# Performance work log

Measured on AMD Instinct MI355X. Metric: run time of the kernel, lower is better.

## Reference

```python
import jax, jax.numpy as jnp
import numpy as np

S, B, MAX_IN, MAX_OUT = 2048, 32, 256, 80
MIN_IN = 20
EPS = 1e-5  # torch BatchNorm1d default


def setup_inputs() -> dict:
    key = jax.random.key(0)
    ks = jax.random.split(key, 4)
    # ragged gene-set sizes per subsystem, and DCell's output-size rule
    in_sizes = jax.random.randint(ks[0], (S,), MIN_IN, MAX_IN + 1)
    out_sizes = jnp.maximum(20, (0.3 * in_sizes).astype(jnp.int32))
    in_mask = (jnp.arange(MAX_IN)[None, :] < in_sizes[:, None]).astype(jnp.float32)   # [S, MAX_IN]
    out_mask = (jnp.arange(MAX_OUT)[None, :] < out_sizes[:, None]).astype(jnp.float32)  # [S, MAX_OUT]
    # gathered mutant states per subsystem (padded), [S, B, MAX_IN]
    x = jax.random.normal(ks[1], (S, B, MAX_IN), dtype=jnp.float32) * in_mask[:, None, :]
    # per-subsystem Linear params (stacked), Kaiming-ish scale
    W = jax.random.normal(ks[2], (S, MAX_OUT, MAX_IN), dtype=jnp.float32) / np.sqrt(MAX_IN).astype(np.float32)
    b = jax.random.normal(ks[3], (S, MAX_OUT), dtype=jnp.float32) * 0.01
    gamma = jnp.ones((S, MAX_OUT), dtype=jnp.float32)
    beta = jnp.zeros((S, MAX_OUT), dtype=jnp.float32)
    return {"x": x, "W": W, "b": b, "gamma": gamma, "beta": beta,
            "in_mask": in_mask, "out_mask": out_mask}


def reference(x, W, b, gamma, beta, in_mask, out_mask):
    # grouped Linear over all subsystems at once: [S,B,I] x [S,O,I] -> [S,B,O]
    xm = x * in_mask[:, None, :]
    h = jnp.einsum('sbi,soi->sbo', xm, W) + b[:, None, :]
    h = jnp.tanh(h)
    # BatchNorm1d (training mode): normalize over the batch dim per subsystem/feature
    mean = jnp.mean(h, axis=1, keepdims=True)
    var = jnp.mean(jnp.square(h - mean), axis=1, keepdims=True)  # biased, as torch BN uses
    y = (h - mean) * jax.lax.rsqrt(var + EPS) * gamma[:, None, :] + beta[:, None, :]
    # zero out padded output features
    return y * out_mask[:, None, :]
```

## Files before the change

kernel.cpp:

```cpp
#include <hip/hip_runtime.h>

#define S_TOT 2048
#define B_SZ  32
#define I_SZ  256
#define O_SZ  80

typedef _Float16 f16x8 __attribute__((ext_vector_type(8)));
typedef _Float16 f16x4 __attribute__((ext_vector_type(4)));
typedef float    f32x4 __attribute__((ext_vector_type(4)));

__global__ __launch_bounds__(320, 5) void dcell_kernel(
    const float* __restrict__ x,
    const float* __restrict__ W,
    const float* __restrict__ bias,
    const float* __restrict__ gamma,
    const float* __restrict__ beta,
    const float* __restrict__ in_mask,
    const float* __restrict__ out_mask,
    float* __restrict__ out)
{
  __shared__ char Xs[16384];

  const int s   = blockIdx.x;
  const int tid = threadIdx.x;

  const float* im = in_mask + (size_t)s * I_SZ;
  float msum = im[0] + im[32] + im[64] + im[96] +
               im[128] + im[160] + im[192] + im[224];
  const int kcmax = (int)(msum + 0.5f);
  const int Kact  = kcmax * 32;

  const int w  = tid >> 6;
  const int l  = tid & 63;
  const int m  = l & 15;
  const int ks = l >> 4;
  const int ob = w * 16;
  const int swz = (m & 7) << 4;

  {
    const float* xg = x + (size_t)s * (B_SZ * I_SZ);
    for (int t = tid; t < (B_SZ * I_SZ) / 4; t += 320) {
      int flat = t * 4;
      int r = flat >> 8, c = flat & 255;
      if (c < Kact) {
        f32x4 v = *(const f32x4*)(xg + flat);
        int off = r * 512 + ((c * 2) ^ ((r & 7) << 4));
        f16x4 h;
        h[0] = (_Float16)v[0]; h[1] = (_Float16)v[1];
        h[2] = (_Float16)v[2]; h[3] = (_Float16)v[3];
        *(f16x4*)(Xs + off) = h;
      }
    }
  }

  f16x8 wf[8];
  {
    const float* wgp = W + ((size_t)s * O_SZ + ob + m) * I_SZ + ks * 8;
#pragma unroll
    for (int kc = 0; kc < 8; ++kc) {
      if (kc < kcmax) {
        f32x4 lo = *(const f32x4*)(wgp + kc * 32);
        f32x4 hi = *(const f32x4*)(wgp + kc * 32 + 4);
        f16x8 h;
        h[0] = (_Float16)lo[0]; h[1] = (_Float16)lo[1];
        h[2] = (_Float16)lo[2]; h[3] = (_Float16)lo[3];
        h[4] = (_Float16)hi[0]; h[5] = (_Float16)hi[1];
        h[6] = (_Float16)hi[2]; h[7] = (_Float16)hi[3];
        wf[kc] = h;
      }
    }
  }
  __syncthreads();

  f32x4 acc0 = {0.f, 0.f, 0.f, 0.f};
  f32x4 acc1 = {0.f, 0.f, 0.f, 0.f};
  const char* xr0 = Xs + m * 512;
  const char* xr1 = Xs + (m + 16) * 512;
#pragma unroll
  for (int kc = 0; kc < 8; ++kc) {
    if (kc < kcmax) {
      int kb = (kc * 64 + ks * 16) ^ swz;
      f16x8 a0 = *(const f16x8*)(xr0 + kb);
      f16x8 a1 = *(const f16x8*)(xr1 + kb);
      acc0 = __builtin_amdgcn_mfma_f32_16x16x32_f16(a0, wf[kc], acc0, 0, 0, 0);
      acc1 = __builtin_amdgcn_mfma_f32_16x16x32_f16(a1, wf[kc], acc1, 0, 0, 0);
    }
  }

  const int o = ob + m;
  const float bv = bias[s * O_SZ + o];
  float t0[4], t1[4];
  float sum = 0.f;
#pragma unroll
  for (int r = 0; r < 4; ++r) {
    t0[r] = tanhf(acc0[r] + bv);
    t1[r] = tanhf(acc1[r] + bv);
    sum += t0[r] + t1[r];
  }
  sum += __shfl_xor(sum, 16);
  sum += __shfl_xor(sum, 32);
  const float mean = sum * (1.0f / 32.0f);

  float vs = 0.f;
#pragma unroll
  for (int r = 0; r < 4; ++r) {
    float d0 = t0[r] - mean, d1 = t1[r] - mean;
    vs += d0 * d0 + d1 * d1;
  }
  vs += __shfl_xor(vs, 16);
  vs += __shfl_xor(vs, 32);
  const float rstd = rsqrtf(vs * (1.0f / 32.0f) + 1e-5f);

  const float g  = gamma[s * O_SZ + o] * rstd;
  const float be = beta[s * O_SZ + o];
  const float om = out_mask[s * O_SZ + o];

  float* og = out + (size_t)s * (B_SZ * O_SZ) + o;
#pragma unroll
  for (int r = 0; r < 4; ++r) {
    int b0 = ks * 4 + r;
    og[(size_t)b0 * O_SZ]        = ((t0[r] - mean) * g + be) * om;
    og[(size_t)(b0 + 16) * O_SZ] = ((t1[r] - mean) * g + be) * om;
  }
}

extern "C" void kernel_launch(void* const* d_in, const int* in_sizes, int n_in,
                              void* d_out, int out_size, void* d_ws, size_t ws_size,
                              hipStream_t stream) {
  const float* x        = (const float*)d_in[0];
  const float* W        = (const float*)d_in[1];
  const float* bias     = (const float*)d_in[2];
  const float* gamma    = (const float*)d_in[3];
  const float* beta     = (const float*)d_in[4];
  const float* in_mask  = (const float*)d_in[5];
  const float* out_mask = (const float*)d_in[6];
  float* out = (float*)d_out;

  dcell_kernel<<<dim3(S_TOT), dim3(320), 0, stream>>>(
      x, W, bias, gamma, beta, in_mask, out_mask, out);
}
```

Measured before the change: 35.70 us.

## Decouple waves from blocks, skip masked output tiles, drop LDS staging

Result: slower. 40.57 us (+13.6%).

```diff
diff --git a/kernel.cpp b/kernel.cpp
--- a/kernel.cpp
+++ b/kernel.cpp
@@ -6,10 +6,23 @@
 #define O_SZ  80
 
 typedef _Float16 f16x8 __attribute__((ext_vector_type(8)));
-typedef _Float16 f16x4 __attribute__((ext_vector_type(4)));
 typedef float    f32x4 __attribute__((ext_vector_type(4)));
 
-__global__ __launch_bounds__(320, 5) void dcell_kernel(
+__device__ __forceinline__ float ftanh(float v) {
+  float e = __expf(2.0f * v);
+  return 1.0f - __fdividef(2.0f, e + 1.0f);
+}
+
+__device__ __forceinline__ f16x8 cvt8(f32x4 lo, f32x4 hi) {
+  f16x8 h;
+  h[0] = (_Float16)lo[0]; h[1] = (_Float16)lo[1];
+  h[2] = (_Float16)lo[2]; h[3] = (_Float16)lo[3];
+  h[4] = (_Float16)hi[0]; h[5] = (_Float16)hi[1];
+  h[6] = (_Float16)hi[2]; h[7] = (_Float16)hi[3];
+  return h;
+}
+
+__global__ __launch_bounds__(256, 6) void dcell_kernel(
     const float* __restrict__ x,
     const float* __restrict__ W,
     const float* __restrict__ bias,
@@ -19,82 +32,67 @@
     const float* __restrict__ out_mask,
     float* __restrict__ out)
 {
-  __shared__ char Xs[16384];
+  const int gw = blockIdx.x * 4 + (threadIdx.x >> 6);
+  const int s  = gw / 5;
+  const int w  = gw - s * 5;
+  const int l  = threadIdx.x & 63;
+  const int m  = l & 15;
+  const int ks = l >> 4;
+  const int ob = w * 16;
+  const int o  = ob + m;
 
-  const int s   = blockIdx.x;
-  const int tid = threadIdx.x;
+  const float* omp = out_mask + (size_t)s * O_SZ;
+  float* og = out + (size_t)s * (B_SZ * O_SZ) + o;
+
+  if (omp[ob] == 0.0f) {
+#pragma unroll
+    for (int r = 0; r < 4; ++r) {
+      int b0 = ks * 4 + r;
+      og[(size_t)b0 * O_SZ]        = 0.f;
+      og[(size_t)(b0 + 16) * O_SZ] = 0.f;
+    }
+    return;
+  }
+  const bool lane_act = (omp[o] != 0.0f);
 
   const float* im = in_mask + (size_t)s * I_SZ;
   float msum = im[0] + im[32] + im[64] + im[96] +
                im[128] + im[160] + im[192] + im[224];
   const int kcmax = (int)(msum + 0.5f);
-  const int Kact  = kcmax * 32;
 
-  const int w  = tid >> 6;
-  const int l  = tid & 63;
-  const int m  = l & 15;
-  const int ks = l >> 4;
-  const int ob = w * 16;
-  const int swz = (m & 7) << 4;
+  const float* xr0 = x + ((size_t)s * B_SZ + m) * I_SZ + ks * 8;
+  const float* xr1 = xr0 + 16 * I_SZ;
+  const float* wr  = W + ((size_t)s * O_SZ + o) * I_SZ + ks * 8;
 
-  {
-    const float* xg = x + (size_t)s * (B_SZ * I_SZ);
-    for (int t = tid; t < (B_SZ * I_SZ) / 4; t += 320) {
-      int flat = t * 4;
-      int r = flat >> 8, c = flat & 255;
-      if (c < Kact) {
-        f32x4 v = *(const f32x4*)(xg + flat);
-        int off = r * 512 + ((c * 2) ^ ((r & 7) << 4));
-        f16x4 h;
-        h[0] = (_Float16)v[0]; h[1] = (_Float16)v[1];
-        h[2] = (_Float16)v[2]; h[3] = (_Float16)v[3];
-        *(f16x4*)(Xs + off) = h;
+  f32x4 acc0 = {0.f, 0.f, 0.f, 0.f};
+  f32x4 acc1 = {0.f, 0.f, 0.f, 0.f};
+#pragma unroll
+  for (int kc = 0; kc < 8; ++kc) {
+    if (kc < kcmax) {
+      f32x4 a0l = *(const f32x4*)(xr0 + kc * 32);
+      f32x4 a0h = *(const f32x4*)(xr0 + kc * 32 + 4);
+      f32x4 a1l = *(const f32x4*)(xr1 + kc * 32);
+      f32x4 a1h = *(const f32x4*)(xr1 + kc * 32 + 4);
+      f16x8 bb = {0, 0, 0, 0, 0, 0, 0, 0};
+      if (lane_act) {
+        f32x4 bl = *(const f32x4*)(wr + kc * 32);
+        f32x4 bh = *(const f32x4*)(wr + kc * 32 + 4);
+        bb = cvt8(bl, bh);
       }
+      f16x8 a0 = cvt8(a0l, a0h);
+      f16x8 a1 = cvt8(a1l, a1h);
+      acc0 = __builtin_amdgcn_mfma_f32_16x16x32_f16(a0, bb, acc0, 0, 0, 0);
+      acc1 = __builtin_amdgcn_mfma_f32_16x16x32_f16(a1, bb, acc1, 0, 0, 0);
     }
   }
 
-  f16x8 wf[8];
-  {
-    const float* wgp = W + ((size_t)s * O_SZ + ob + m) * I_SZ + ks * 8;
-#pragma unroll
-    for (int kc = 0; kc < 8; ++kc) {
-      if (kc < kcmax) {
-        f32x4 lo = *(const f32x4*)(wgp + kc * 32);
-        f32x4 hi = *(const f32x4*)(wgp + kc * 32 + 4);
-        f16x8 h;
-        h[0] = (_Float16)lo[0]; h[1] = (_Float16)lo[1];
-        h[2] = (_Float16)lo[2]; h[3] = (_Float16)lo[3];
-        h[4] = (_Float16)hi[0]; h[5] = (_Float16)hi[1];
-        h[6] = (_Float16)hi[2]; h[7] = (_Float16)hi[3];
-        wf[kc] = h;
-      }
-    }
-  }
-  __syncthreads();
-
-  f32x4 acc0 = {0.f, 0.f, 0.f, 0.f};
-  f32x4 acc1 = {0.f, 0.f, 0.f, 0.f};
-  const char* xr0 = Xs + m * 512;
-  const char* xr1 = Xs + (m + 16) * 512;
-#pragma unroll
-  for (int kc = 0; kc < 8; ++kc) {
-    if (kc < kcmax) {
-      int kb = (kc * 64 + ks * 16) ^ swz;
-      f16x8 a0 = *(const f16x8*)(xr0 + kb);
-      f16x8 a1 = *(const f16x8*)(xr1 + kb);
-      acc0 = __builtin_amdgcn_mfma_f32_16x16x32_f16(a0, wf[kc], acc0, 0, 0, 0);
-      acc1 = __builtin_amdgcn_mfma_f32_16x16x32_f16(a1, wf[kc], acc1, 0, 0, 0);
-    }
-  }
-
-  const int o = ob + m;
   const float bv = bias[s * O_SZ + o];
   float t0[4], t1[4];
   float sum = 0.f;
 #pragma unroll
   for (int r = 0; r < 4; ++r) {
-    t0[r] = tanhf(acc0[r] + bv);
-    t1[r] = tanhf(acc1[r] + bv);
+    t0[r] = ftanh(acc0[r] + bv);
+    t1[r] = ftanh(acc1[r] + bv);
     sum += t0[r] + t1[r];
   }
   sum += __shfl_xor(sum, 16);
@@ -113,9 +111,8 @@
 
   const float g  = gamma[s * O_SZ + o] * rstd;
   const float be = beta[s * O_SZ + o];
-  const float om = out_mask[s * O_SZ + o];
+  const float om = omp[o];
 
-  float* og = out + (size_t)s * (B_SZ * O_SZ) + o;
 #pragma unroll
   for (int r = 0; r < 4; ++r) {
     int b0 = ks * 4 + r;
@@ -136,6 +133,6 @@
   const float* out_mask = (const float*)d_in[6];
   float* out = (float*)d_out;
 
-  dcell_kernel<<<dim3(S_TOT), dim3(320), 0, stream>>>(
+  dcell_kernel<<<dim3((S_TOT * 5) / 4), dim3(256), 0, stream>>>(
       x, W, bias, gamma, beta, in_mask, out_mask, out);
 }
```
